# Kernel tuning notes

Measured on AMD Instinct MI355X. Metric: run time of the kernel, lower is better.

## Reference

```python
import jax, jax.numpy as jnp
import numpy as np

N, E, D_IN, H = 40000, 640000, 128, 128
R, B = 8, 30  # num_relations = 2*n_speakers**2, num_bases


def setup_inputs() -> dict:
    key = jax.random.key(0)
    ks = jax.random.split(key, 10)
    node_features = jax.random.normal(ks[0], (N, D_IN), jnp.float32)
    edge_index = jax.random.randint(ks[1], (2, E), 0, N)
    edge_type = jax.random.randint(ks[2], (E,), 0, R)
    edge_norm = jax.random.uniform(ks[3], (E,), jnp.float32)
    s_in = 1.0 / np.sqrt(D_IN)
    s_h = 1.0 / np.sqrt(H)
    basis = jax.random.normal(ks[4], (B, D_IN, H), jnp.float32) * s_in
    comp = jax.random.normal(ks[5], (R, B), jnp.float32) * (1.0 / np.sqrt(B))
    root = jax.random.normal(ks[6], (D_IN, H), jnp.float32) * s_in
    bias1 = jnp.zeros((H,), jnp.float32)
    w_rel = jax.random.normal(ks[7], (H, H), jnp.float32) * s_h
    w_root2 = jax.random.normal(ks[8], (H, H), jnp.float32) * s_h
    bias2 = jnp.zeros((H,), jnp.float32)
    return dict(node_features=node_features, edge_index=edge_index,
                edge_norm=edge_norm, edge_type=edge_type,
                basis=basis, comp=comp, root=root, bias1=bias1,
                w_rel=w_rel, w_root2=w_root2, bias2=bias2)


def reference(node_features, edge_index, edge_norm, edge_type,
              basis, comp, root, bias1, w_rel, w_root2, bias2):
    n = node_features.shape[0]
    src, dst = edge_index[0], edge_index[1]  # messages flow src -> dst

    # ---- RGCNConv (basis decomposition, mean aggregation, root + bias) ----
    # Per-relation weights from bases: [R, D_in, H]
    w = jnp.einsum('rb,bio->rio', comp, basis)
    # Transform all nodes by every relation once (avoids per-edge matmul): [R, N, H]
    xw = jnp.einsum('nd,rdo->rno', node_features, w)
    msgs = xw[edge_type, src]                                  # [E, H]
    agg = jax.ops.segment_sum(msgs, dst, num_segments=n)       # [N, H]
    deg = jax.ops.segment_sum(jnp.ones_like(dst, dtype=node_features.dtype),
                              dst, num_segments=n)
    agg = agg / jnp.maximum(deg, 1.0)[:, None]                 # mean aggregation
    h = agg + node_features @ root + bias1                     # [N, H]

    # ---- GraphConv (add aggregation): W_rel * sum_j x_j + W_root * x_i + b ----
    nbr = jax.ops.segment_sum(h[src], dst, num_segments=n)     # [N, H]
    out = nbr @ w_rel + h @ w_root2 + bias2
    return out
```

## Files before the change

kernel.cpp:

```cpp
#include <hip/hip_runtime.h>
#include <stdint.h>

#define DH 128
#define NB 30
#define NR 8

typedef short bf16x8 __attribute__((ext_vector_type(8)));
typedef float f32x4 __attribute__((ext_vector_type(4)));
typedef float f32x2 __attribute__((ext_vector_type(2)));

static __device__ __forceinline__ unsigned short f2bf(float f) {
    unsigned u = __float_as_uint(f);
    u += 0x7fffu + ((u >> 16) & 1u);
    return (unsigned short)(u >> 16);
}
static __device__ __forceinline__ float bflo(unsigned u) { return __uint_as_float(u << 16); }
static __device__ __forceinline__ float bfhi(unsigned u) { return __uint_as_float(u & 0xffff0000u); }


__global__ __launch_bounds__(256) void k_prephist(const float* __restrict__ comp,
                                                  const float* __restrict__ basis,
                                                  const float* __restrict__ root,
                                                  const float* __restrict__ wrel,
                                                  const float* __restrict__ wroot2,
                                                  unsigned short* __restrict__ wallT,
                                                  unsigned short* __restrict__ WT2,
                                                  const int* __restrict__ dstA, int E,
                                                  int* __restrict__ deg,
                                                  int* __restrict__ rank, int histB) {
    int b = blockIdx.x;
    int tid = threadIdx.x;
    if (b < histB) {
        int e = b * 256 + tid;
        if (e < E) rank[e] = atomicAdd(&deg[dstA[e]], 1);
        return;
    }
    int unit = (b - histB) * 2 + (tid >> 7);
    int o = tid & 127;
    int i = unit & 127;
    int y = unit >> 7;
    if (y < NR) {
        float s = 0.f;
        #pragma unroll
        for (int bb = 0; bb < NB; ++bb)
            s += comp[y * NB + bb] * basis[((size_t)bb * DH + i) * DH + o];
        wallT[((size_t)y * DH + o) * DH + i] = f2bf(s);
    } else if (y == NR) {
        wallT[((size_t)NR * DH + o) * DH + i] = f2bf(root[i * DH + o]);
    } else {
        const float* W = (y == NR + 2) ? wroot2 : wrel;
        int id = (i & 7) * 16 + (i >> 3);
        WT2[((size_t)(y - NR - 1) * DH + o) * DH + i] = f2bf(W[(size_t)id * DH + o]);
    }
}

__global__ __launch_bounds__(1024) void k_scan(const int* __restrict__ deg, int n, int total_n,
                                               int* __restrict__ offsets,
                                               unsigned long long* __restrict__ st,
                                               int* __restrict__ ticket) {
    __shared__ int s[1024];
    __shared__ int bid_s, pre_s;
    const int tid = threadIdx.x;
    if (tid == 0) bid_s = atomicAdd(ticket, 1);
    __syncthreads();
    const int b = bid_s;
    const int base = b * 4096 + tid * 4;
    int v[4];
    #pragma unroll
    for (int j = 0; j < 4; ++j) {
        int i = base + j;
        v[j] = (i < n) ? deg[i] : 0;
    }
    int tsum = v[0] + v[1] + v[2] + v[3];
    s[tid] = tsum;
    __syncthreads();
    for (int off = 1; off < 1024; off <<= 1) {
        int t = (tid >= off) ? s[tid - off] : 0;
        __syncthreads();
        s[tid] += t;
        __syncthreads();
    }
    if (tid == 0) {
        int total = s[1023];
        atomicExch(&st[b], (1ULL << 62) | (unsigned long long)(unsigned)total);
        long long pre = 0;
        int t = b - 1;
        while (t >= 0) {
            unsigned long long w;
            do { w = atomicAdd(&st[t], 0ULL); } while (w == 0ULL);
            pre += (long long)(w & 0x3FFFFFFFFFFFFFFFULL);
            if ((w >> 62) == 2ULL) break;
            --t;
        }
        atomicExch(&st[b], (2ULL << 62) | (unsigned long long)(pre + total));
        pre_s = (int)pre;
    }
    __syncthreads();
    int run = pre_s + s[tid] - tsum;
    #pragma unroll
    for (int j = 0; j < 4; ++j) {
        int i = base + j;
        if (i < total_n) offsets[i] = run;
        run += v[j];
    }
}

__global__ __launch_bounds__(512, 4) void k_gemm1s(const float* __restrict__ x,
                                                   const unsigned short* __restrict__ wallT,
                                                   const float* __restrict__ bias1,
                                                   int Nn,
                                                   unsigned* __restrict__ xw8,
                                                   unsigned short* __restrict__ hb,
                                                   const int* __restrict__ src,
                                                   const int* __restrict__ dstA,
                                                   const int* __restrict__ etype, int E,
                                                   const int* __restrict__ offsets,
                                                   const int* __restrict__ rank,
                                                   unsigned* __restrict__ sorted,
                                                   int scatB, int gx) {
    __shared__ __align__(16) unsigned short As[128][136];
    __shared__ __align__(16) unsigned short Bs[128][136];
    const int tid = threadIdx.x;
    const int b = blockIdx.x;

    const bool is_scat = (b < 2 * scatB) && (b & 1);

    if (is_scat) {
        const int sidx = b >> 1;
        const int stride = scatB * 512;
        for (int e = sidx * 512 + tid; e < E; e += stride) {
            int d = dstA[e];
            int pos = offsets[d] + rank[e];
            sorted[pos] = (unsigned)src[e] | ((unsigned)etype[e] << 17);
        }
        return;
    }

    const int bg = (b < 2 * scatB) ? (b >> 1) : (b - scatB);
    const int wave = tid >> 6, lane = tid & 63;
    const int g = bg / gx;
    const int rowbase = (bg % gx) * 128;
    const int lq = lane >> 4, lr = lane & 15;

    #pragma unroll
    for (int it = 0; it < 4; ++it) {
        int c = it * 512 + tid;
        int row = c >> 4, col = c & 15;
        int rg = rowbase + row; if (rg >= Nn) rg = Nn - 1;
        float4 v0 = *(const float4*)&x[(size_t)rg * DH + col * 8];
        float4 v1 = *(const float4*)&x[(size_t)rg * DH + col * 8 + 4];
        uint4 u;
        u.x = (unsigned)f2bf(v0.x) | ((unsigned)f2bf(v0.y) << 16);
        u.y = (unsigned)f2bf(v0.z) | ((unsigned)f2bf(v0.w) << 16);
        u.z = (unsigned)f2bf(v1.x) | ((unsigned)f2bf(v1.y) << 16);
        u.w = (unsigned)f2bf(v1.z) | ((unsigned)f2bf(v1.w) << 16);
        *(uint4*)&As[row][col * 8] = u;
    }

    for (int rr = 0; rr < 3; ++rr) {
        const int r = g * 3 + rr;
        const unsigned short* WT = wallT + (size_t)r * DH * DH;
        if (rr) __syncthreads();
        #pragma unroll
        for (int it = 0; it < 4; ++it) {
            int c = it * 512 + tid;
            int row = c >> 4, col = c & 15;
            *(uint4*)&Bs[row][col * 8] = *(const uint4*)&WT[(size_t)row * DH + col * 8];
        }
        __syncthreads();

        f32x4 acc[8];
        #pragma unroll
        for (int nt = 0; nt < 8; ++nt) acc[nt] = (f32x4)0.f;

        #pragma unroll
        for (int ks = 0; ks < 4; ++ks) {
            const int ko = ks * 32 + lq * 8;
            bf16x8 a0 = *(const bf16x8*)&As[wave * 16 + lr][ko];
            #pragma unroll
            for (int nt = 0; nt < 8; ++nt) {
                bf16x8 bb = *(const bf16x8*)&Bs[nt * 16 + lr][ko];
                acc[nt] = __builtin_amdgcn_mfma_f32_16x16x32_bf16(a0, bb, acc[nt], 0, 0, 0);
            }
        }
        if (r < NR) {
            unsigned* dst = xw8 + ((size_t)r * Nn + rowbase) * (DH / 4);
            #pragma unroll
            for (int reg = 0; reg < 4; ++reg) {
                int m = wave * 16 + lq * 4 + reg;
                if (rowbase + m < Nn) {
                    uint2 o;
                    o.x = __builtin_amdgcn_cvt_pk_fp8_f32(acc[0][reg], acc[1][reg], 0, false);
                    o.x = __builtin_amdgcn_cvt_pk_fp8_f32(acc[2][reg], acc[3][reg], o.x, true);
                    o.y = __builtin_amdgcn_cvt_pk_fp8_f32(acc[4][reg], acc[5][reg], 0, false);
                    o.y = __builtin_amdgcn_cvt_pk_fp8_f32(acc[6][reg], acc[7][reg], o.y, true);
                    *(uint2*)&dst[(size_t)m * (DH / 4) + lr * 2] = o;
                }
            }
        } else {
            float bv[8];
            #pragma unroll
            for (int nt = 0; nt < 8; ++nt) bv[nt] = bias1[nt * 16 + lr];
            #pragma unroll
            for (int reg = 0; reg < 4; ++reg) {
                int m = rowbase + wave * 16 + lq * 4 + reg;
                if (m < Nn) {
                    uint4 u;
                    u.x = (unsigned)f2bf(acc[0][reg] + bv[0]) | ((unsigned)f2bf(acc[1][reg] + bv[1]) << 16);
                    u.y = (unsigned)f2bf(acc[2][reg] + bv[2]) | ((unsigned)f2bf(acc[3][reg] + bv[3]) << 16);
                    u.z = (unsigned)f2bf(acc[4][reg] + bv[4]) | ((unsigned)f2bf(acc[5][reg] + bv[5]) << 16);
                    u.w = (unsigned)f2bf(acc[6][reg] + bv[6]) | ((unsigned)f2bf(acc[7][reg] + bv[7]) << 16);
                    *(uint4*)&hb[(size_t)m * DH + lr * 8] = u;
                }
            }
        }
    }
}

__global__ __launch_bounds__(256) void k_agg1(const int* __restrict__ offsets,
                                              const unsigned* __restrict__ sorted,
                                              const unsigned* __restrict__ xw8,
                                              const unsigned* __restrict__ hb32,
                                              int Nn, unsigned* __restrict__ hbf) {
    int w = (blockIdx.x * blockDim.x + threadIdx.x) >> 6;
    if (w >= Nn) return;
    int lane = threadIdx.x & 63;
    int half = lane >> 5, sub = lane & 31;
    int s = offsets[w], e = offsets[w + 1];
    float a0 = 0.f, a1 = 0.f, a2 = 0.f, a3 = 0.f;
    int p = s;
    for (; p + 16 <= e; p += 16) {
        unsigned pk[8];
        #pragma unroll
        for (int j = 0; j < 8; ++j) pk[j] = sorted[p + 2 * j + half];
        unsigned u[8];
        #pragma unroll
        for (int j = 0; j < 8; ++j)
            u[j] = xw8[((size_t)(pk[j] >> 17) * Nn + (pk[j] & 0x1FFFFu)) * 32 + sub];
        #pragma unroll
        for (int j = 0; j < 8; ++j) {
            f32x2 lo = __builtin_amdgcn_cvt_pk_f32_fp8(u[j], false);
            f32x2 hi = __builtin_amdgcn_cvt_pk_f32_fp8(u[j], true);
            a0 += lo.x; a1 += lo.y; a2 += hi.x; a3 += hi.y;
        }
    }
    if (p < e) {
        unsigned pk[8]; float m[8];
        #pragma unroll
        for (int j = 0; j < 8; ++j) {
            int q = p + 2 * j + half; bool v = q < e;
            pk[j] = sorted[v ? q : e - 1];
            m[j] = v ? 1.f : 0.f;
        }
        unsigned u[8];
        #pragma unroll
        for (int j = 0; j < 8; ++j)
            u[j] = xw8[((size_t)(pk[j] >> 17) * Nn + (pk[j] & 0x1FFFFu)) * 32 + sub];
        #pragma unroll
        for (int j = 0; j < 8; ++j) {
            f32x2 lo = __builtin_amdgcn_cvt_pk_f32_fp8(u[j], false);
            f32x2 hi = __builtin_amdgcn_cvt_pk_f32_fp8(u[j], true);
            a0 = fmaf(m[j], lo.x, a0);
            a1 = fmaf(m[j], lo.y, a1);
            a2 = fmaf(m[j], hi.x, a2);
            a3 = fmaf(m[j], hi.y, a3);
        }
    }
    a0 += __shfl_xor(a0, 32, 64);
    a1 += __shfl_xor(a1, 32, 64);
    a2 += __shfl_xor(a2, 32, 64);
    a3 += __shfl_xor(a3, 32, 64);
    if (half == 0) {
        float invd = 1.0f / fmaxf((float)(e - s), 1.0f);
        uint2 hv = *(const uint2*)&hb32[(size_t)w * 64 + sub * 2];
        float h0 = bflo(hv.x) + a0 * invd;
        float h1 = bfhi(hv.x) + a1 * invd;
        float h2 = bflo(hv.y) + a2 * invd;
        float h3 = bfhi(hv.y) + a3 * invd;
        uint2 o;
        o.x = (unsigned)f2bf(h0) | ((unsigned)f2bf(h1) << 16);
        o.y = (unsigned)f2bf(h2) | ((unsigned)f2bf(h3) << 16);
        *(uint2*)&hbf[(size_t)w * 64 + sub * 2] = o;
    }
}

__global__ __launch_bounds__(256, 3) void k_gemm2d(const unsigned short* __restrict__ hbf,
                                                   const unsigned short* __restrict__ WT2,
                                                   const float* __restrict__ bias2,
                                                   int Nn,
                                                   unsigned short* __restrict__ hw,
                                                   unsigned short* __restrict__ hro) {
    __shared__ __align__(16) unsigned short As[64][136];
    __shared__ __align__(16) unsigned short Bs[128][136];
    const int tid = threadIdx.x;
    const int wave = tid >> 6, lane = tid & 63;
    const int rowbase = blockIdx.x * 64;
    const int lq = lane >> 4, lr = lane & 15;

    #pragma unroll
    for (int it = 0; it < 4; ++it) {
        int c = it * 256 + tid;
        int row = c >> 4, col = c & 15;
        int rg = rowbase + row; if (rg >= Nn) rg = Nn - 1;
        *(uint4*)&As[row][col * 8] = *(const uint4*)&hbf[(size_t)rg * DH + col * 8];
    }

    for (int ph = 0; ph < 2; ++ph) {
        const unsigned short* WT = WT2 + (size_t)ph * DH * DH;
        if (ph) __syncthreads();
        #pragma unroll
        for (int it = 0; it < 8; ++it) {
            int c = it * 256 + tid;
            int row = c >> 4, col = c & 15;
            *(uint4*)&Bs[row][col * 8] = *(const uint4*)&WT[(size_t)row * DH + col * 8];
        }
        __syncthreads();

        f32x4 acc[8];
        #pragma unroll
        for (int nt = 0; nt < 8; ++nt) acc[nt] = (f32x4)0.f;

        #pragma unroll
        for (int ks = 0; ks < 4; ++ks) {
            const int ko = ks * 32 + lq * 8;
            bf16x8 a0 = *(const bf16x8*)&As[wave * 16 + lr][ko];
            #pragma unroll
            for (int nt = 0; nt < 8; ++nt) {
                bf16x8 bb = *(const bf16x8*)&Bs[nt * 16 + lr][ko];
                acc[nt] = __builtin_amdgcn_mfma_f32_16x16x32_bf16(a0, bb, acc[nt], 0, 0, 0);
            }
        }
        __syncthreads();

        float bv[8];
        #pragma unroll
        for (int nt = 0; nt < 8; ++nt) bv[nt] = ph ? bias2[nt * 16 + lr] : 0.f;
        #pragma unroll
        for (int nt = 0; nt < 8; ++nt)
            #pragma unroll
            for (int reg = 0; reg < 4; ++reg) {
                int ml = wave * 16 + lq * 4 + reg;
                Bs[ml][nt * 16 + lr] = f2bf(acc[nt][reg] + bv[nt]);
            }
        __syncthreads();

        unsigned short* dst = ph ? hro : hw;
        #pragma unroll
        for (int it = 0; it < 4; ++it) {
            int c = it * 256 + tid;
            int row = c >> 4, col = c & 15;
            if (rowbase + row < Nn)
                *(uint4*)&dst[(size_t)(rowbase + row) * DH + col * 8] = *(uint4*)&Bs[row][col * 8];
        }
    }
}

__global__ __launch_bounds__(256) void k_aggout(const int* __restrict__ offsets,
                                                const unsigned* __restrict__ sorted,
                                                const uint2* __restrict__ hw2,
                                                const uint2* __restrict__ hro2,
                                                int Nn, float* __restrict__ out) {
    int w = (blockIdx.x * blockDim.x + threadIdx.x) >> 6;
    if (w >= Nn) return;
    int lane = threadIdx.x & 63;
    int half = lane >> 5, sub = lane & 31;
    int s = offsets[w], e = offsets[w + 1];
    float a0 = 0.f, a1 = 0.f, a2 = 0.f, a3 = 0.f;
    int p = s;
    for (; p + 16 <= e; p += 16) {
        unsigned pk[8];
        #pragma unroll
        for (int j = 0; j < 8; ++j) pk[j] = sorted[p + 2 * j + half];
        uint2 u[8];
        #pragma unroll
        for (int j = 0; j < 8; ++j)
            u[j] = hw2[(size_t)(pk[j] & 0x1FFFFu) * 32 + sub];
        #pragma unroll
        for (int j = 0; j < 8; ++j) {
            a0 += bflo(u[j].x); a1 += bfhi(u[j].x);
            a2 += bflo(u[j].y); a3 += bfhi(u[j].y);
        }
    }
    if (p < e) {
        unsigned pk[8]; float m[8];
        #pragma unroll
        for (int j = 0; j < 8; ++j) {
            int q = p + 2 * j + half; bool v = q < e;
            pk[j] = sorted[v ? q : e - 1];
            m[j] = v ? 1.f : 0.f;
        }
        uint2 u[8];
        #pragma unroll
        for (int j = 0; j < 8; ++j)
            u[j] = hw2[(size_t)(pk[j] & 0x1FFFFu) * 32 + sub];
        #pragma unroll
        for (int j = 0; j < 8; ++j) {
            a0 = fmaf(m[j], bflo(u[j].x), a0);
            a1 = fmaf(m[j], bfhi(u[j].x), a1);
            a2 = fmaf(m[j], bflo(u[j].y), a2);
            a3 = fmaf(m[j], bfhi(u[j].y), a3);
        }
    }
    a0 += __shfl_xor(a0, 32, 64);
    a1 += __shfl_xor(a1, 32, 64);
    a2 += __shfl_xor(a2, 32, 64);
    a3 += __shfl_xor(a3, 32, 64);
    if (half == 0) {
        uint2 hv = hro2[(size_t)w * 32 + sub];
        float4 o;
        o.x = a0 + bflo(hv.x);
        o.y = a1 + bfhi(hv.x);
        o.z = a2 + bflo(hv.y);
        o.w = a3 + bfhi(hv.y);
        *(float4*)&out[(size_t)w * DH + sub * 4] = o;
    }
}

extern "C" void kernel_launch(void* const* d_in, const int* in_sizes, int n_in,
                              void* d_out, int out_size, void* d_ws, size_t ws_size,
                              hipStream_t stream) {
    const float* x      = (const float*)d_in[0];
    const int*   eidx   = (const int*)d_in[1];
    const int*   etype  = (const int*)d_in[3];
    const float* basis  = (const float*)d_in[4];
    const float* comp   = (const float*)d_in[5];
    const float* root   = (const float*)d_in[6];
    const float* bias1  = (const float*)d_in[7];
    const float* wrel   = (const float*)d_in[8];
    const float* wroot2 = (const float*)d_in[9];
    const float* bias2  = (const float*)d_in[10];
    float* out = (float*)d_out;

    const int N = in_sizes[0] / DH;
    const int E = in_sizes[3];
    const int* srcA = eidx;
    const int* dstA = eidx + E;

    char* ws = (char*)d_ws;
    size_t off = 0;
    auto alloc = [&](size_t bytes) -> void* {
        void* p = (void*)(ws + off);
        off += (bytes + 255) & ~(size_t)255;
        return p;
    };
    int* deg           = (int*)alloc((size_t)N * 4);
    unsigned long long* st = (unsigned long long*)alloc(64 * 8);
    int* ticket        = (int*)alloc(256);
    int* rank          = (int*)alloc((size_t)E * 4);
    int* offsets       = (int*)alloc((size_t)(N + 1) * 4);
    unsigned* sorted   = (unsigned*)alloc((size_t)E * 4);
    unsigned short* wallT = (unsigned short*)alloc((size_t)(NR + 1) * DH * DH * 2);
    unsigned short* WT2   = (unsigned short*)alloc((size_t)2 * DH * DH * 2);
    unsigned* xw8      = (unsigned*)alloc((size_t)NR * N * DH);
    unsigned short* hb = (unsigned short*)alloc((size_t)N * DH * 2);
    unsigned* hbf      = (unsigned*)alloc((size_t)N * (DH / 2) * 4);
    unsigned short* hw  = (unsigned short*)alloc((size_t)N * DH * 2);
    unsigned short* hro = (unsigned short*)alloc((size_t)N * DH * 2);
    (void)ws_size; (void)n_in; (void)out_size;

    hipMemsetAsync(deg, 0, (size_t)N * 4 + 768, stream);

    const int histB = (E + 255) / 256;
    k_prephist<<<histB + 704, 256, 0, stream>>>(comp, basis, root, wrel, wroot2,
                                                wallT, WT2, dstA, E, deg, rank, histB);

    const int totn = N + 1;
    const int nsb = (totn + 4095) / 4096;
    k_scan<<<nsb, 1024, 0, stream>>>(deg, N, totn, offsets, st, ticket);

    const int gx = (N + 127) / 128;
    const int gemmB = gx * 3;
    const int scatB = 640;
    k_gemm1s<<<scatB + gemmB, 512, 0, stream>>>(x, wallT, bias1, N, xw8, hb,
                                                srcA, dstA, etype, E, offsets, rank, sorted,
                                                scatB, gx);

    k_agg1<<<(N * 64) / 256, 256, 0, stream>>>(offsets, sorted, xw8,
                                               (const unsigned*)hb, N, hbf);
    k_gemm2d<<<(N + 63) / 64, 256, 0, stream>>>((const unsigned short*)hbf, WT2, bias2, N, hw, hro);
    k_aggout<<<(N * 64) / 256, 256, 0, stream>>>(offsets, sorted, (const uint2*)hw,
                                                 (const uint2*)hro, N, out);
}
```

Before: 220.4 us.

## Prefetch relation weights via direct global-to-LDS loads and enlarge gemm2 tiles

In the first GEMM, weight tiles are now stored XOR-swizzled in global memory and copied straight into unpadded LDS with global_load_lds. The next relation's tile is prefetched while the current epilogue runs, which removes the register round-trip and overlaps the weight fetch with the stores. The second GEMM moves from 64-row tiles with 256 threads to 128-row tiles with 512 threads, halving the number of times its weights are loaded. The swizzle is there to avoid LDS bank conflicts without padding. The risk is that the in-flight async LDS writes and the epilogue must be ordered correctly by the barriers.

```diff
diff --git a/kernel.cpp b/kernel.cpp
--- a/kernel.cpp
+++ b/kernel.cpp
@@ -16,6 +16,12 @@
 }
 static __device__ __forceinline__ float bflo(unsigned u) { return __uint_as_float(u << 16); }
 static __device__ __forceinline__ float bfhi(unsigned u) { return __uint_as_float(u & 0xffff0000u); }
+
+static __device__ __forceinline__ void gl_lds16(const void* g, void* l) {
+    __builtin_amdgcn_global_load_lds((const __attribute__((address_space(1))) unsigned int*)g,
+                                     (__attribute__((address_space(3))) unsigned int*)l,
+                                     16, 0, 0);
+}
 
 
 __global__ __launch_bounds__(256) void k_prephist(const float* __restrict__ comp,
@@ -39,14 +45,15 @@
     int o = tid & 127;
     int i = unit & 127;
     int y = unit >> 7;
+    int iswz = ((((i >> 3) ^ (o & 7)) << 3) | (i & 7));
     if (y < NR) {
         float s = 0.f;
         #pragma unroll
         for (int bb = 0; bb < NB; ++bb)
             s += comp[y * NB + bb] * basis[((size_t)bb * DH + i) * DH + o];
-        wallT[((size_t)y * DH + o) * DH + i] = f2bf(s);
+        wallT[((size_t)y * DH + o) * DH + iswz] = f2bf(s);
     } else if (y == NR) {
-        wallT[((size_t)NR * DH + o) * DH + i] = f2bf(root[i * DH + o]);
+        wallT[((size_t)NR * DH + o) * DH + iswz] = f2bf(root[i * DH + o]);
     } else {
         const float* W = (y == NR + 2) ? wroot2 : wrel;
         int id = (i & 7) * 16 + (i >> 3);
@@ -119,7 +126,7 @@
                                                    unsigned* __restrict__ sorted,
                                                    int scatB, int gx) {
     __shared__ __align__(16) unsigned short As[128][136];
-    __shared__ __align__(16) unsigned short Bs[128][136];
+    __shared__ __align__(16) unsigned short BsL[128 * 128];
     const int tid = threadIdx.x;
     const int b = blockIdx.x;
 
@@ -157,16 +164,17 @@
         *(uint4*)&As[row][col * 8] = u;
     }
 
+    {
+        const unsigned short* w0 = wallT + (size_t)(g * 3) * DH * DH;
+        #pragma unroll
+        for (int it = 0; it < 4; ++it) {
+            int c = it * 512 + tid;
+            gl_lds16(w0 + (size_t)c * 8, &BsL[(size_t)(it * 512 + (tid & ~63)) * 8]);
+        }
+    }
+
     for (int rr = 0; rr < 3; ++rr) {
         const int r = g * 3 + rr;
-        const unsigned short* WT = wallT + (size_t)r * DH * DH;
-        if (rr) __syncthreads();
-        #pragma unroll
-        for (int it = 0; it < 4; ++it) {
-            int c = it * 512 + tid;
-            int row = c >> 4, col = c & 15;
-            *(uint4*)&Bs[row][col * 8] = *(const uint4*)&WT[(size_t)row * DH + col * 8];
-        }
         __syncthreads();
 
         f32x4 acc[8];
@@ -179,10 +187,23 @@
             bf16x8 a0 = *(const bf16x8*)&As[wave * 16 + lr][ko];
             #pragma unroll
             for (int nt = 0; nt < 8; ++nt) {
-                bf16x8 bb = *(const bf16x8*)&Bs[nt * 16 + lr][ko];
+                const int row = nt * 16 + lr;
+                const int gph = (ks * 4 + lq) ^ (row & 7);
+                bf16x8 bb = *(const bf16x8*)&BsL[row * 128 + gph * 8];
                 acc[nt] = __builtin_amdgcn_mfma_f32_16x16x32_bf16(a0, bb, acc[nt], 0, 0, 0);
             }
         }
+        __syncthreads();
+
+        if (rr < 2) {
+            const unsigned short* wn = wallT + (size_t)(r + 1) * DH * DH;
+            #pragma unroll
+            for (int it = 0; it < 4; ++it) {
+                int c = it * 512 + tid;
+                gl_lds16(wn + (size_t)c * 8, &BsL[(size_t)(it * 512 + (tid & ~63)) * 8]);
+            }
+        }
+
         if (r < NR) {
             unsigned* dst = xw8 + ((size_t)r * Nn + rowbase) * (DH / 4);
             #pragma unroll
@@ -284,22 +305,22 @@
     }
 }
 
-__global__ __launch_bounds__(256, 3) void k_gemm2d(const unsigned short* __restrict__ hbf,
+__global__ __launch_bounds__(512, 4) void k_gemm2d(const unsigned short* __restrict__ hbf,
                                                    const unsigned short* __restrict__ WT2,
                                                    const float* __restrict__ bias2,
                                                    int Nn,
                                                    unsigned short* __restrict__ hw,
                                                    unsigned short* __restrict__ hro) {
-    __shared__ __align__(16) unsigned short As[64][136];
+    __shared__ __align__(16) unsigned short As[128][136];
     __shared__ __align__(16) unsigned short Bs[128][136];
     const int tid = threadIdx.x;
     const int wave = tid >> 6, lane = tid & 63;
-    const int rowbase = blockIdx.x * 64;
+    const int rowbase = blockIdx.x * 128;
     const int lq = lane >> 4, lr = lane & 15;
 
     #pragma unroll
     for (int it = 0; it < 4; ++it) {
-        int c = it * 256 + tid;
+        int c = it * 512 + tid;
         int row = c >> 4, col = c & 15;
         int rg = rowbase + row; if (rg >= Nn) rg = Nn - 1;
         *(uint4*)&As[row][col * 8] = *(const uint4*)&hbf[(size_t)rg * DH + col * 8];
@@ -309,8 +330,8 @@
         const unsigned short* WT = WT2 + (size_t)ph * DH * DH;
         if (ph) __syncthreads();
         #pragma unroll
-        for (int it = 0; it < 8; ++it) {
-            int c = it * 256 + tid;
+        for (int it = 0; it < 4; ++it) {
+            int c = it * 512 + tid;
             int row = c >> 4, col = c & 15;
             *(uint4*)&Bs[row][col * 8] = *(const uint4*)&WT[(size_t)row * DH + col * 8];
         }
@@ -347,7 +368,7 @@
         unsigned short* dst = ph ? hro : hw;
         #pragma unroll
         for (int it = 0; it < 4; ++it) {
-            int c = it * 256 + tid;
+            int c = it * 512 + tid;
             int row = c >> 4, col = c & 15;
             if (rowbase + row < Nn)
                 *(uint4*)&dst[(size_t)(rowbase + row) * DH + col * 8] = *(uint4*)&Bs[row][col * 8];
@@ -477,7 +498,7 @@
 
     k_agg1<<<(N * 64) / 256, 256, 0, stream>>>(offsets, sorted, xw8,
                                                (const unsigned*)hb, N, hbf);
-    k_gemm2d<<<(N + 63) / 64, 256, 0, stream>>>((const unsigned short*)hbf, WT2, bias2, N, hw, hro);
+    k_gemm2d<<<gx, 512, 0, stream>>>((const unsigned short*)hbf, WT2, bias2, N, hw, hro);
     k_aggout<<<(N * 64) / 256, 256, 0, stream>>>(offsets, sorted, (const uint2*)hw,
                                                  (const uint2*)hro, N, out);
 }
```

Measured after the change: 221.3 us. Within noise of the previous version (+0.4%).
